# Kernel tuning notes

Hardware: AMD Instinct MI355X
Metric: run time of the kernel (lower is better)

## Reference

```python
import jax, jax.numpy as jnp
import numpy as np

B, S, D = 8, 2048, 512

def setup_inputs() -> dict:
    key = jax.random.key(0)
    k1, k2 = jax.random.split(key)
    x = jax.random.normal(k1, (B, S, D), dtype=jnp.float32)
    # nn.Parameter(torch.rand(D, D)) -> uniform [0, 1)
    attn_matrix = jax.random.uniform(k2, (D, D), dtype=jnp.float32)
    return {"x": x, "attn_matrix": attn_matrix}

def reference(x, attn_matrix):
    # scalar = sqrt(last dim of x)
    scale = jnp.sqrt(jnp.asarray(x.shape[-1], dtype=x.dtype))
    # prod = x @ W @ x^T / sqrt(D)  -> [B, S, S]
    xw = jnp.einsum('bsd,de->bse', x, attn_matrix)
    prod = jnp.einsum('bse,bte->bst', xw, x) / scale
    scores = jax.nn.softmax(prod, axis=-1)
    out = jnp.einsum('bst,btd->bsd', scores, x)
    return out
```

## Files before the change

### kernel.cpp

```cpp
#include <hip/hip_runtime.h>
#include <math.h>

#define B_ 8
#define S_ 2048
#define D_ 512
#define HSZ (B_ * S_ * D_)

typedef _Float16 half8 __attribute__((ext_vector_type(8)));
typedef _Float16 half4h __attribute__((ext_vector_type(4)));
typedef __fp16 fp16x2 __attribute__((ext_vector_type(2)));
typedef float f32x4 __attribute__((ext_vector_type(4)));
typedef float f32x16 __attribute__((ext_vector_type(16)));
typedef unsigned int u32;
typedef u32 u32x4 __attribute__((ext_vector_type(4)));

constexpr float INV_SCALE = 0.044194173824159216f;

__device__ __forceinline__ u32 pk16(float a, float b) {
    fp16x2 r = __builtin_amdgcn_cvt_pkrtz(a, b);
    union { fp16x2 h; u32 u; } U; U.h = r; return U.u;
}

__global__ __launch_bounds__(256) void cvtW(const float* __restrict__ W,
                                            _Float16* __restrict__ WT) {
    __shared__ float T[64 * 65];
    const int tid = threadIdx.x;
    const int r = blockIdx.x;
    const int t0 = (r >> 3) * 64, d0 = (r & 7) * 64;

#pragma unroll
    for (int it = 0; it < 4; ++it) {
        int flat = it * 256 + tid;
        int row = flat >> 4, c4 = (flat & 15) * 4;
        float4 v = *(const float4*)(W + (size_t)(t0 + row) * 512 + d0 + c4);
        T[row * 65 + c4 + 0] = v.x; T[row * 65 + c4 + 1] = v.y;
        T[row * 65 + c4 + 2] = v.z; T[row * 65 + c4 + 3] = v.w;
    }
    __syncthreads();
#pragma unroll
    for (int it = 0; it < 2; ++it) {
        int flat = it * 256 + tid;
        int d = flat >> 3, c = (flat & 7) * 8;
        half8 hv;
#pragma unroll
        for (int j = 0; j < 8; ++j) hv[j] = (_Float16)T[(c + j) * 65 + d];
        int n = d0 + d, k = t0 + c;
        int off = ((n >> 5) << 14) | ((k >> 4) << 9) | ((n & 31) << 4) |
                  (((k >> 3) & 1) << 3) | (k & 7);
        *(half8*)(WT + off) = hv;
    }
}

__global__ __launch_bounds__(256, 2)
void gemmF(const float* __restrict__ x, const _Float16* __restrict__ WT,
           _Float16* __restrict__ xK, _Float16* __restrict__ xV,
           _Float16* __restrict__ qwh) {
    __shared__ float T[32 * 516];
    const int tid = threadIdx.x;
    const int w = tid >> 6, lane = tid & 63;
    const int r31 = lane & 31, hi = lane >> 5;
    const int laneoff = (r31 << 4) + (hi << 3);
    const int blk = blockIdx.x;
    const int b = blk & 7;
    const int mt = blk >> 3;
    const size_t bb = (size_t)b * (S_ * D_);

    {
        const float* xs = x + bb + (size_t)(mt * 32) * 512;
#pragma unroll
        for (int it = 0; it < 16; ++it) {
            int f = it * 256 + tid;
            int row = f >> 7, c4 = (f & 127) << 2;
            float4 v = *(const float4*)(xs + (size_t)row * 512 + c4);
            *(float4*)&T[row * 516 + c4] = v;
        }
    }
    __syncthreads();

    {
        _Float16* xvb = xV + bb + ((size_t)mt << 14) + (w << 12);
#pragma unroll
        for (int dc = 0; dc < 4; ++dc)
#pragma unroll
            for (int kh = 0; kh < 2; ++kh) {
                int d = w * 128 + dc * 32 + r31;
                half8 v;
#pragma unroll
                for (int j = 0; j < 8; ++j)
                    v[j] = (_Float16)T[(kh * 16 + hi * 8 + j) * 516 + d];
                *(half8*)(xvb + (dc << 10) + (kh << 9) + laneoff) = v;
            }
    }

    f32x16 acc[4];
#pragma unroll
    for (int nt = 0; nt < 4; ++nt)
#pragma unroll
        for (int r = 0; r < 16; ++r) acc[nt][r] = 0.f;

    const _Float16* wtb = WT + ((w * 4) << 14) + laneoff;
    _Float16* xkb = xK + bb + ((size_t)mt << 14);

    for (int ph = 0; ph < 2; ++ph) {
        half8 A[16];
#pragma unroll
        for (int kc8 = 0; kc8 < 16; ++kc8) {
            int kc = ph * 16 + kc8;
            const float* tr = &T[r31 * 516 + kc * 16 + hi * 8];
            half8 a;
#pragma unroll
            for (int j = 0; j < 8; ++j) a[j] = (_Float16)tr[j];
            A[kc8] = a;
            if ((kc & 3) == w)
                *(half8*)(xkb + (kc << 9) + laneoff) = a;
        }
#pragma unroll
        for (int kc8 = 0; kc8 < 16; ++kc8) {
            int kc = ph * 16 + kc8;
            half8 B0 = *(const half8*)(wtb + (0 << 14) + (kc << 9));
            half8 B1 = *(const half8*)(wtb + (1 << 14) + (kc << 9));
            half8 B2 = *(const half8*)(wtb + (2 << 14) + (kc << 9));
            half8 B3 = *(const half8*)(wtb + (3 << 14) + (kc << 9));
            acc[0] = __builtin_amdgcn_mfma_f32_32x32x16_f16(A[kc8], B0, acc[0], 0, 0, 0);
            acc[1] = __builtin_amdgcn_mfma_f32_32x32x16_f16(A[kc8], B1, acc[1], 0, 0, 0);
            acc[2] = __builtin_amdgcn_mfma_f32_32x32x16_f16(A[kc8], B2, acc[2], 0, 0, 0);
            acc[3] = __builtin_amdgcn_mfma_f32_32x32x16_f16(A[kc8], B3, acc[3], 0, 0, 0);
        }
    }

    __syncthreads();

    {
        float* tw = T + w * 1152;
        const int mm = lane >> 1, kkg = lane & 1;
        _Float16* qb2 = qwh + bb + ((size_t)mt << 14) + (w << 12) +
                        (mm << 4) + (kkg << 3);
#pragma unroll
        for (int nt = 0; nt < 4; ++nt) {
#pragma unroll
            for (int r = 0; r < 16; ++r) {
                int mrow = (r & 3) + ((r >> 2) << 3) + (hi << 2);
                tw[mrow * 36 + r31] = acc[nt][r] * INV_SCALE;
            }
#pragma unroll
            for (int c8 = 0; c8 < 2; ++c8) {
                const float* tr2 = tw + mm * 36 + c8 * 16 + kkg * 8;
                f32x4 a = *(const f32x4*)(tr2);
                f32x4 bq = *(const f32x4*)(tr2 + 4);
                u32x4 st = { pk16(a[0], a[1]), pk16(a[2], a[3]),
                             pk16(bq[0], bq[1]), pk16(bq[2], bq[3]) };
                *(u32x4*)(qb2 + ((nt * 2 + c8) << 9)) = st;
            }
        }
    }
}

__global__ __launch_bounds__(256, 2)
void flashP(const _Float16* __restrict__ xK, const _Float16* __restrict__ xV,
            const _Float16* __restrict__ qwh, float* __restrict__ out) {
    __shared__ __align__(16) unsigned char SMEM[34816];
    float* Sx = (float*)SMEM;

    const int tid = threadIdx.x;
    const int w = tid >> 6, lane = tid & 63;
    const int r31 = lane & 31, hi = lane >> 5;
    const int laneoff = (r31 << 4) + (hi << 3);
    const int d0w = w * 128;
    const int bx = blockIdx.x;
    const int b = bx & 7;
    const int q0 = (bx >> 3) * 32;
    const size_t xb = (size_t)b * (S_ * D_);

    half8 Qr[8];
    {
        const _Float16* qb = qwh + xb + ((q0 >> 5) << 14) + (w << 12) + laneoff;
#pragma unroll
        for (int kc = 0; kc < 8; ++kc)
            Qr[kc] = *(const half8*)(qb + (kc << 9));
    }

    const _Float16* kbase = xK + xb + (w << 12) + laneoff;
    const _Float16* vbase = xV + xb + (w << 12) + laneoff;

    half8 KA[8], KB[8];
    f32x16 sS;

#pragma unroll
    for (int kc = 0; kc < 8; ++kc)
        KA[kc] = *(const half8*)(kbase + (kc << 9));
    {
        f32x16 s;
#pragma unroll
        for (int r = 0; r < 16; ++r) s[r] = 0.f;
#pragma unroll
        for (int kc = 0; kc < 8; ++kc)
            s = __builtin_amdgcn_mfma_f32_32x32x16_f16(KA[kc], Qr[kc], s, 0, 0, 0);
        sS = s;
    }
#pragma unroll
    for (int kc = 0; kc < 8; ++kc)
        KB[kc] = *(const half8*)(kbase + (1 << 14) + (kc << 9));
    {
        float* sxw = Sx + w * 1024;
#pragma unroll
        for (int r2 = 0; r2 < 4; ++r2) {
            f32x4 v_ = { sS[4 * r2 + 0], sS[4 * r2 + 1], sS[4 * r2 + 2], sS[4 * r2 + 3] };
            *(f32x4*)&sxw[(r2 * 64 + lane) * 4] = v_;
        }
    }
    __syncthreads();

    f32x16 O[4];
#pragma unroll
    for (int dc = 0; dc < 4; ++dc)
#pragma unroll
        for (int r = 0; r < 16; ++r) O[dc][r] = 0.f;
    float m = -1e30f, l = 0.f;

#define SMX_HEAD(TI) \
    half8 Vc[8]; \
    _Pragma("unroll") for (int dc = 0; dc < 4; ++dc) \
    _Pragma("unroll") for (int kh = 0; kh < 2; ++kh) \
        Vc[dc * 2 + kh] = *(const half8*)(vbase + ((TI) << 14) + (dc << 10) + (kh << 9)); \
    float sv[16]; \
    { \
        _Pragma("unroll") for (int i = 0; i < 16; ++i) sv[i] = sS[i]; \
        _Pragma("unroll") for (int pw = 1; pw < 4; ++pw) { \
            const float* sxp = Sx + (((TI) & 1) * 4 + (w ^ pw)) * 1024; \
            _Pragma("unroll") for (int r2 = 0; r2 < 4; ++r2) { \
                f32x4 pp = *(const f32x4*)&sxp[(r2 * 64 + lane) * 4]; \
                _Pragma("unroll") for (int j = 0; j < 4; ++j) sv[4 * r2 + j] += pp[j]; \
            } \
        } \
    } \
    float mt_ = sv[0]; \
    _Pragma("unroll") for (int i = 1; i < 16; ++i) mt_ = fmaxf(mt_, sv[i]); \
    mt_ = fmaxf(mt_, __shfl_xor(mt_, 32)); \
    if (__any(mt_ > m + 8.f)) { \
        float mn = fmaxf(m, mt_); \
        float a_ = __expf(m - mn); \
        l *= a_; \
        _Pragma("unroll") for (int dc = 0; dc < 4; ++dc) \
        _Pragma("unroll") for (int r = 0; r < 16; ++r) O[dc][r] *= a_; \
        m = mn; \
    } \
    float pa[16]; float rs = 0.f; \
    _Pragma("unroll") for (int i = 0; i < 16; ++i) { pa[i] = __expf(sv[i] - m); rs += pa[i]; } \
    l += rs + __shfl_xor(rs, 32);

#define SMX_TAILPART \
    u32 q16[8]; \
    _Pragma("unroll") for (int r2 = 0; r2 < 4; ++r2) { \
        q16[2 * r2 + 0] = pk16(pa[4 * r2 + 0], pa[4 * r2 + 1]); \
        q16[2 * r2 + 1] = pk16(pa[4 * r2 + 2], pa[4 * r2 + 3]); \
    } \
    half8 Pf[2]; \
    _Pragma("unroll") for (int kh = 0; kh < 2; ++kh) { \
        int r2o = 2 * kh + hi, r2s = 2 * kh + (hi ^ 1); \
        u32 rv0 = (u32)__shfl_xor((int)q16[2 * r2s + 0], 32); \
        u32 rv1 = (u32)__shfl_xor((int)q16[2 * r2s + 1], 32); \
        u32 o0 = q16[2 * r2o + 0], o1 = q16[2 * r2o + 1]; \
        union { u32 u[4]; half8 v; } U_; \
        U_.u[0] = hi ? rv0 : o0; U_.u[1] = hi ? rv1 : o1; \
        U_.u[2] = hi ? o0 : rv0; U_.u[3] = hi ? o1 : rv1; \
        Pf[kh] = U_.v; \
    } \
    _Pragma("unroll") for (int dc = 0; dc < 4; ++dc) { \
        O[dc] = __builtin_amdgcn_mfma_f32_32x32x16_f16(Vc[dc * 2 + 0], Pf[0], O[dc], 0, 0, 0); \
        O[dc] = __builtin_amdgcn_mfma_f32_32x32x16_f16(Vc[dc * 2 + 1], Pf[1], O[dc], 0, 0, 0); \
    }

#define PBODY(TI, KRD, KWR) do {                                                \
    SMX_HEAD(TI)                                                                \
                 \
    f32x16 sn_;                                                                 \
    {                                                                           \
        f32x16 s_;                                                              \
        _Pragma("unroll") for (int r = 0; r < 16; ++r) s_[r] = 0.f;             \
        _Pragma("unroll") for (int kc = 0; kc < 8; ++kc)                        \
            s_ = __builtin_amdgcn_mfma_f32_32x32x16_f16(KRD[kc], Qr[kc], s_, 0, 0, 0); \
        sn_ = s_;                                                               \
    }                                                                           \
                                   \
    {                                                                           \
        const int tp2_ = ((TI) + 2) & 63;                                       \
        _Pragma("unroll") for (int kc = 0; kc < 8; ++kc)                        \
            KWR[kc] = *(const half8*)(kbase + (tp2_ << 14) + (kc << 9));        \
    }                                                                           \
    SMX_TAILPART                                                                \
    sS = sn_;                                                                   \
    {                                                                           \
        float* sxw = Sx + ((((TI) + 1) & 1) * 4 + w) * 1024;                    \
        _Pragma("unroll") for (int r2 = 0; r2 < 4; ++r2) {                      \
            f32x4 v_ = { sS[4 * r2 + 0], sS[4 * r2 + 1], sS[4 * r2 + 2], sS[4 * r2 + 3] }; \
            *(f32x4*)&sxw[(r2 * 64 + lane) * 4] = v_;                           \
        }                                                                       \
    }                                                                           \
    __syncthreads();                                                            \
} while (0)

    for (int tp = 0; tp < 31; ++tp) {
        PBODY(2 * tp,     KB, KA);
        PBODY(2 * tp + 1, KA, KB);
    }
    PBODY(62, KB, KA);
    {
        SMX_HEAD(63)
        SMX_TAILPART
    }
#undef PBODY
#undef SMX_HEAD
#undef SMX_TAILPART

    __syncthreads();

    {
        float inv = 1.0f / l;
        float* ew = (float*)SMEM + w * 2176;
        const int qq = lane >> 1, cs = (lane & 1) * 32;
#pragma unroll
        for (int ph = 0; ph < 2; ++ph) {
#pragma unroll
            for (int dc = 0; dc < 2; ++dc)
#pragma unroll
                for (int r = 0; r < 16; ++r) {
                    int dl = dc * 32 + (r & 3) + ((r >> 2) << 3) + (hi << 2);
                    ew[r31 * 68 + dl] = O[ph * 2 + dc][r] * inv;
                }
            float* gp = out + xb + (size_t)(q0 + qq) * 512 + d0w + ph * 64 + cs;
#pragma unroll
            for (int k = 0; k < 8; ++k)
                *(f32x4*)(gp + 4 * k) = *(const f32x4*)&ew[qq * 68 + cs + 4 * k];
        }
    }
}

__global__ __launch_bounds__(256) void xw_gemm_f32(const float* __restrict__ A,
                                                   const float* __restrict__ W,
                                                   float* __restrict__ C) {
    __shared__ float As[16][65];
    __shared__ float Bs[16][64];
    const int tid = threadIdx.x;
    const int row0 = blockIdx.y * 64, col0 = blockIdx.x * 64;
    const int ty = tid / 16, tx = tid % 16;
    float acc[4][4] = {};
    const int ar = tid / 4, ak = (tid % 4) * 4, bk = tid / 16, bn = (tid % 16) * 4;
    for (int k0 = 0; k0 < 512; k0 += 16) {
        float4 a4 = *(const float4*)(A + (size_t)(row0 + ar) * 512 + k0 + ak);
        float4 b4 = *(const float4*)(W + (size_t)(k0 + bk) * 512 + col0 + bn);
        __syncthreads();
        As[ak + 0][ar] = a4.x; As[ak + 1][ar] = a4.y;
        As[ak + 2][ar] = a4.z; As[ak + 3][ar] = a4.w;
        *(float4*)&Bs[bk][bn] = b4;
        __syncthreads();
#pragma unroll
        for (int kk = 0; kk < 16; kk++) {
            float a[4], bv[4];
#pragma unroll
            for (int i = 0; i < 4; i++) a[i] = As[kk][ty * 4 + i];
#pragma unroll
            for (int j = 0; j < 4; j++) bv[j] = Bs[kk][tx * 4 + j];
#pragma unroll
            for (int i = 0; i < 4; i++)
#pragma unroll
                for (int j = 0; j < 4; j++) acc[i][j] += a[i] * bv[j];
        }
    }
#pragma unroll
    for (int i = 0; i < 4; i++) {
        float4 o = make_float4(acc[i][0] * INV_SCALE, acc[i][1] * INV_SCALE,
                               acc[i][2] * INV_SCALE, acc[i][3] * INV_SCALE);
        *(float4*)(C + (size_t)(row0 + ty * 4 + i) * 512 + col0 + tx * 4) = o;
    }
}

__global__ __launch_bounds__(256) void flash_f32(const float* __restrict__ x,
                                                 const float* __restrict__ qw,
                                                 float* __restrict__ out) {
    __shared__ float4 kt[16 * 136];
    const int tid = threadIdx.x;
    const int q = tid >> 3, g = tid & 7;
    const int blk = blockIdx.x;
    const int b = blk >> 6;
    const int qrow = (blk & 63) * 32 + q;
    const size_t xbase = (size_t)b * S_ * D_;
    float qwr[64];
    {
        const float4* p = (const float4*)(qw + xbase + (size_t)qrow * D_ + g * 64);
#pragma unroll
        for (int i4 = 0; i4 < 16; i4++) {
            float4 v = p[i4];
            qwr[4 * i4 + 0] = v.x; qwr[4 * i4 + 1] = v.y;
            qwr[4 * i4 + 2] = v.z; qwr[4 * i4 + 3] = v.w;
        }
    }
    float oa[64];
#pragma unroll
    for (int i = 0; i < 64; i++) oa[i] = 0.f;
    float m = -1e30f, l = 0.f;
    const float4* x4 = (const float4*)(x + xbase);
    for (int t0 = 0; t0 < S_; t0 += 16) {
        __syncthreads();
#pragma unroll
        for (int j = 0; j < 8; j++) {
            int f = tid + j * 256;
            int tt = f >> 7, c = f & 127;
            kt[tt * 136 + (c >> 4) * 17 + (c & 15)] = x4[(size_t)(t0 + tt) * 128 + c];
        }
        __syncthreads();
#pragma unroll 1
        for (int tt = 0; tt < 16; tt++) {
            float4 kv[16];
            const float4* kp = &kt[tt * 136 + g * 17];
#pragma unroll
            for (int i4 = 0; i4 < 16; i4++) kv[i4] = kp[i4];
            float s = 0.f;
#pragma unroll
            for (int i4 = 0; i4 < 16; i4++)
                s += qwr[4 * i4] * kv[i4].x + qwr[4 * i4 + 1] * kv[i4].y
                   + qwr[4 * i4 + 2] * kv[i4].z + qwr[4 * i4 + 3] * kv[i4].w;
            s += __shfl_xor(s, 1, 64); s += __shfl_xor(s, 2, 64); s += __shfl_xor(s, 4, 64);
            if (s > m) {
                float alpha = __expf(m - s);
                l *= alpha;
#pragma unroll
                for (int i = 0; i < 64; i++) oa[i] *= alpha;
                m = s;
            }
            float p = __expf(s - m);
            l += p;
#pragma unroll
            for (int i4 = 0; i4 < 16; i4++) {
                oa[4 * i4 + 0] += p * kv[i4].x; oa[4 * i4 + 1] += p * kv[i4].y;
                oa[4 * i4 + 2] += p * kv[i4].z; oa[4 * i4 + 3] += p * kv[i4].w;
            }
        }
    }
    float inv_l = 1.0f / l;
    float4* op = (float4*)(out + xbase + (size_t)qrow * D_ + g * 64);
#pragma unroll
    for (int i4 = 0; i4 < 16; i4++)
        op[i4] = make_float4(oa[4 * i4] * inv_l, oa[4 * i4 + 1] * inv_l,
                             oa[4 * i4 + 2] * inv_l, oa[4 * i4 + 3] * inv_l);
}

extern "C" void kernel_launch(void* const* d_in, const int* in_sizes, int n_in,
                              void* d_out, int out_size, void* d_ws, size_t ws_size,
                              hipStream_t stream) {
    const float* x = (const float*)d_in[0];
    const float* W = (const float*)d_in[1];
    float* out = (float*)d_out;

    const size_t F16 = (size_t)HSZ * sizeof(_Float16);
    const size_t off_qwh = 0;
    const size_t off_xK  = F16;
    const size_t off_xV  = 2 * F16;
    const size_t off_WT  = 3 * F16;
    const size_t base    = 3 * F16 + 512 * 512 * sizeof(_Float16);

    if (ws_size >= base) {
        _Float16* qwh = (_Float16*)((char*)d_ws + off_qwh);
        _Float16* xK  = (_Float16*)((char*)d_ws + off_xK);
        _Float16* xV  = (_Float16*)((char*)d_ws + off_xV);
        _Float16* WT  = (_Float16*)((char*)d_ws + off_WT);

        cvtW<<<64, 256, 0, stream>>>(W, WT);
        gemmF<<<512, 256, 0, stream>>>(x, WT, xK, xV, qwh);
        flashP<<<512, 256, 0, stream>>>(xK, xV, qwh, out);
    } else {
        const size_t needf = (size_t)HSZ * sizeof(float);
        float* xw = (ws_size >= needf) ? (float*)d_ws : out;
        dim3 g1(512 / 64, (B_ * S_) / 64);
        xw_gemm_f32<<<g1, 256, 0, stream>>>(x, W, xw);
        flash_f32<<<B_ * (S_ / 32), 256, 0, stream>>>(x, xw, out);
    }
}
```

Baseline: 227.4 us.

## Fuse x@W projection into flash attention kernel prologue, drop qwh buffer

The x@W GEMM moves out of the conversion kernel and into the start of the flash kernel. Each block now computes its own 32-row Q tile in registers from the fp16 x tile and the transposed W, which removes the qwh workspace write and its read-back. The conversion kernel now only emits the fp16 K and V layouts. The cost is a longer prologue in the flash kernel and extra register pressure there, which may affect occupancy.

Result: no change. 229.8 us (+1.1%).

```diff
diff --git a/kernel.cpp b/kernel.cpp
--- a/kernel.cpp
+++ b/kernel.cpp
@@ -52,9 +52,8 @@
 }
 
 __global__ __launch_bounds__(256, 2)
-void gemmF(const float* __restrict__ x, const _Float16* __restrict__ WT,
-           _Float16* __restrict__ xK, _Float16* __restrict__ xV,
-           _Float16* __restrict__ qwh) {
+void cvtX(const float* __restrict__ x, _Float16* __restrict__ xK,
+          _Float16* __restrict__ xV) {
     __shared__ float T[32 * 516];
     const int tid = threadIdx.x;
     const int w = tid >> 6, lane = tid & 63;
@@ -92,72 +91,23 @@
             }
     }
 
-    f32x16 acc[4];
-#pragma unroll
-    for (int nt = 0; nt < 4; ++nt)
-#pragma unroll
-        for (int r = 0; r < 16; ++r) acc[nt][r] = 0.f;
-
-    const _Float16* wtb = WT + ((w * 4) << 14) + laneoff;
-    _Float16* xkb = xK + bb + ((size_t)mt << 14);
-
-    for (int ph = 0; ph < 2; ++ph) {
-        half8 A[16];
-#pragma unroll
-        for (int kc8 = 0; kc8 < 16; ++kc8) {
-            int kc = ph * 16 + kc8;
+    {
+        _Float16* xkb = xK + bb + ((size_t)mt << 14);
+#pragma unroll
+        for (int k8 = 0; k8 < 8; ++k8) {
+            int kc = k8 * 4 + w;
             const float* tr = &T[r31 * 516 + kc * 16 + hi * 8];
             half8 a;
 #pragma unroll
             for (int j = 0; j < 8; ++j) a[j] = (_Float16)tr[j];
-            A[kc8] = a;
-            if ((kc & 3) == w)
-                *(half8*)(xkb + (kc << 9) + laneoff) = a;
-        }
-#pragma unroll
-        for (int kc8 = 0; kc8 < 16; ++kc8) {
-            int kc = ph * 16 + kc8;
-            half8 B0 = *(const half8*)(wtb + (0 << 14) + (kc << 9));
-            half8 B1 = *(const half8*)(wtb + (1 << 14) + (kc << 9));
-            half8 B2 = *(const half8*)(wtb + (2 << 14) + (kc << 9));
-            half8 B3 = *(const half8*)(wtb + (3 << 14) + (kc << 9));
-            acc[0] = __builtin_amdgcn_mfma_f32_32x32x16_f16(A[kc8], B0, acc[0], 0, 0, 0);
-            acc[1] = __builtin_amdgcn_mfma_f32_32x32x16_f16(A[kc8], B1, acc[1], 0, 0, 0);
-            acc[2] = __builtin_amdgcn_mfma_f32_32x32x16_f16(A[kc8], B2, acc[2], 0, 0, 0);
-            acc[3] = __builtin_amdgcn_mfma_f32_32x32x16_f16(A[kc8], B3, acc[3], 0, 0, 0);
-        }
-    }
-
-    __syncthreads();
-
-    {
-        float* tw = T + w * 1152;
-        const int mm = lane >> 1, kkg = lane & 1;
-        _Float16* qb2 = qwh + bb + ((size_t)mt << 14) + (w << 12) +
-                        (mm << 4) + (kkg << 3);
-#pragma unroll
-        for (int nt = 0; nt < 4; ++nt) {
-#pragma unroll
-            for (int r = 0; r < 16; ++r) {
-                int mrow = (r & 3) + ((r >> 2) << 3) + (hi << 2);
-                tw[mrow * 36 + r31] = acc[nt][r] * INV_SCALE;
-            }
-#pragma unroll
-            for (int c8 = 0; c8 < 2; ++c8) {
-                const float* tr2 = tw + mm * 36 + c8 * 16 + kkg * 8;
-                f32x4 a = *(const f32x4*)(tr2);
-                f32x4 bq = *(const f32x4*)(tr2 + 4);
-                u32x4 st = { pk16(a[0], a[1]), pk16(a[2], a[3]),
-                             pk16(bq[0], bq[1]), pk16(bq[2], bq[3]) };
-                *(u32x4*)(qb2 + ((nt * 2 + c8) << 9)) = st;
-            }
+            *(half8*)(xkb + (kc << 9) + laneoff) = a;
         }
     }
 }
 
 __global__ __launch_bounds__(256, 2)
-void flashP(const _Float16* __restrict__ xK, const _Float16* __restrict__ xV,
-            const _Float16* __restrict__ qwh, float* __restrict__ out) {
+void flashF(const _Float16* __restrict__ xK, const _Float16* __restrict__ xV,
+            const _Float16* __restrict__ WT, float* __restrict__ out) {
     __shared__ __align__(16) unsigned char SMEM[34816];
     float* Sx = (float*)SMEM;
 
@@ -171,16 +121,58 @@
     const int q0 = (bx >> 3) * 32;
     const size_t xb = (size_t)b * (S_ * D_);
 
-    half8 Qr[8];
-    {
-        const _Float16* qb = qwh + xb + ((q0 >> 5) << 14) + (w << 12) + laneoff;
-#pragma unroll
-        for (int kc = 0; kc < 8; ++kc)
-            Qr[kc] = *(const half8*)(qb + (kc << 9));
-    }
-
     const _Float16* kbase = xK + xb + (w << 12) + laneoff;
     const _Float16* vbase = xV + xb + (w << 12) + laneoff;
+
+    half8 Qr[8];
+    {
+        const _Float16* aq = xK + xb + ((size_t)(q0 >> 5) << 14) + laneoff;
+        const _Float16* wtb = WT + ((w * 4) << 14) + laneoff;
+        f32x16 acc[4];
+#pragma unroll
+        for (int nt = 0; nt < 4; ++nt)
+#pragma unroll
+            for (int r = 0; r < 16; ++r) acc[nt][r] = 0.f;
+#pragma unroll
+        for (int kg = 0; kg < 4; ++kg) {
+            half8 Ax[8];
+#pragma unroll
+            for (int k8 = 0; k8 < 8; ++k8)
+                Ax[k8] = *(const half8*)(aq + ((kg * 8 + k8) << 9));
+#pragma unroll
+            for (int k8 = 0; k8 < 8; ++k8) {
+                int kc = kg * 8 + k8;
+                half8 B0 = *(const half8*)(wtb + (0 << 14) + (kc << 9));
+                half8 B1 = *(const half8*)(wtb + (1 << 14) + (kc << 9));
+                half8 B2 = *(const half8*)(wtb + (2 << 14) + (kc << 9));
+                half8 B3 = *(const half8*)(wtb + (3 << 14) + (kc << 9));
+                acc[0] = __builtin_amdgcn_mfma_f32_32x32x16_f16(Ax[k8], B0, acc[0], 0, 0, 0);
+                acc[1] = __builtin_amdgcn_mfma_f32_32x32x16_f16(Ax[k8], B1, acc[1], 0, 0, 0);
+                acc[2] = __builtin_amdgcn_mfma_f32_32x32x16_f16(Ax[k8], B2, acc[2], 0, 0, 0);
+                acc[3] = __builtin_amdgcn_mfma_f32_32x32x16_f16(Ax[k8], B3, acc[3], 0, 0, 0);
+            }
+        }
+        float* tw = (float*)SMEM + w * 1152;
+#pragma unroll
+        for (int nt = 0; nt < 4; ++nt) {
+#pragma unroll
+            for (int r = 0; r < 16; ++r) {
+                int mrow = (r & 3) + ((r >> 2) << 3) + (hi << 2);
+                tw[mrow * 36 + r31] = acc[nt][r] * INV_SCALE;
+            }
+#pragma unroll
+            for (int h2 = 0; h2 < 2; ++h2) {
+                const float* tr = tw + r31 * 36 + h2 * 16 + hi * 8;
+                f32x4 a = *(const f32x4*)(tr);
+                f32x4 b4 = *(const f32x4*)(tr + 4);
+                half8 q;
+#pragma unroll
+                for (int j = 0; j < 4; ++j) { q[j] = (_Float16)a[j]; q[4 + j] = (_Float16)b4[j]; }
+                Qr[2 * nt + h2] = q;
+            }
+        }
+    }
+    __syncthreads();
 
     half8 KA[8], KB[8];
     f32x16 sS;
@@ -272,7 +264,6 @@
 
 #define PBODY(TI, KRD, KWR) do {                                                \
     SMX_HEAD(TI)                                                                \
-                 \
     f32x16 sn_;                                                                 \
     {                                                                           \
         f32x16 s_;                                                              \
@@ -281,7 +272,6 @@
             s_ = __builtin_amdgcn_mfma_f32_32x32x16_f16(KRD[kc], Qr[kc], s_, 0, 0, 0); \
         sn_ = s_;                                                               \
     }                                                                           \
-                                   \
     {                                                                           \
         const int tp2_ = ((TI) + 2) & 63;                                       \
         _Pragma("unroll") for (int kc = 0; kc < 8; ++kc)                        \
@@ -452,21 +442,19 @@
     float* out = (float*)d_out;
 
     const size_t F16 = (size_t)HSZ * sizeof(_Float16);
-    const size_t off_qwh = 0;
-    const size_t off_xK  = F16;
-    const size_t off_xV  = 2 * F16;
-    const size_t off_WT  = 3 * F16;
-    const size_t base    = 3 * F16 + 512 * 512 * sizeof(_Float16);
+    const size_t off_xK = 0;
+    const size_t off_xV = F16;
+    const size_t off_WT = 2 * F16;
+    const size_t base   = 2 * F16 + 512 * 512 * sizeof(_Float16);
 
     if (ws_size >= base) {
-        _Float16* qwh = (_Float16*)((char*)d_ws + off_qwh);
-        _Float16* xK  = (_Float16*)((char*)d_ws + off_xK);
-        _Float16* xV  = (_Float16*)((char*)d_ws + off_xV);
-        _Float16* WT  = (_Float16*)((char*)d_ws + off_WT);
+        _Float16* xK = (_Float16*)((char*)d_ws + off_xK);
+        _Float16* xV = (_Float16*)((char*)d_ws + off_xV);
+        _Float16* WT = (_Float16*)((char*)d_ws + off_WT);
 
         cvtW<<<64, 256, 0, stream>>>(W, WT);
-        gemmF<<<512, 256, 0, stream>>>(x, WT, xK, xV, qwh);
-        flashP<<<512, 256, 0, stream>>>(xK, xV, qwh, out);
+        cvtX<<<512, 256, 0, stream>>>(x, xK, xV);
+        flashF<<<512, 256, 0, stream>>>(xK, xV, WT, out);
     } else {
         const size_t needf = (size_t)HSZ * sizeof(float);
         float* xw = (ws_size >= needf) ? (float*)d_ws : out;
```
